# Kernel tuning notes

Measured on AMD Instinct MI355X. Metric: run time of the kernel, lower is better.

## Reference

```python
import jax, jax.numpy as jnp
import numpy as np

N_SAMPLES = 4194304
N_RAYS = 131072


def setup_inputs() -> dict:
    key = jax.random.key(0)
    k1, k2, k3, k4, k5, k6 = jax.random.split(key, 6)
    alpha = jax.random.uniform(k1, (N_SAMPLES, 1), dtype=jnp.float32)
    values3d = jax.random.uniform(k2, (N_SAMPLES, 3), dtype=jnp.float32)
    values1d = jax.random.uniform(k3, (N_SAMPLES, 1), dtype=jnp.float32)
    weights = jax.random.uniform(k4, (N_SAMPLES, 1), dtype=jnp.float32)
    sample_values = jax.random.normal(k5, (N_SAMPLES, 3), dtype=jnp.float32)
    ray_id = jnp.sort(jax.random.randint(k6, (N_SAMPLES,), 0, N_RAYS, dtype=jnp.int32))
    return {"alpha": alpha, "values3d": values3d, "values1d": values1d,
            "weights": weights, "sample_values": sample_values,
            "ray_id": ray_id, "n_rays": N_RAYS}


def _transmittance(alpha, ray_id, n_rays):
    # exclusive cumprod of (1 - alpha) within each packed ray segment, in log space
    logs = jnp.log(jnp.clip(1.0 - alpha[:, 0], 1e-7, 1.0))          # [N]
    csum = jnp.cumsum(logs)
    excl = csum - logs                                               # exclusive cumsum
    first = jnp.concatenate([jnp.ones((1,), bool), ray_id[1:] != ray_id[:-1]])
    seg_base = jax.ops.segment_sum(jnp.where(first, excl, 0.0), ray_id,
                                   num_segments=n_rays)              # [R]
    transmittance = jnp.exp(excl - seg_base[ray_id])[:, None]        # [N,1]
    bg_transmittance = jnp.exp(jax.ops.segment_sum(logs, ray_id,
                                                   num_segments=n_rays))  # [R]
    return transmittance, bg_transmittance


def reference(alpha, values3d, values1d, weights, sample_values, ray_id, n_rays):
    transmittance, bg_transmittance = _transmittance(alpha, ray_id, n_rays)
    # integrate_3d / integrate_1d: per-ray sum of value * weight
    integrated_3d = jax.ops.segment_sum(values3d * weights, ray_id, num_segments=n_rays)  # [R,3]
    integrated_1d = jax.ops.segment_sum(values1d * weights, ray_id, num_segments=n_rays)  # [R,1]
    # SumOverRay: per-ray sum plus broadcast back to each sample
    sum_per_ray = jax.ops.segment_sum(sample_values, ray_id, num_segments=n_rays)         # [R,3]
    sum_per_sample = sum_per_ray[ray_id]                                                  # [N,3]
    return (transmittance, bg_transmittance, integrated_3d, integrated_1d,
            sum_per_ray, sum_per_sample)
```

## Files before the change

### kernel.cpp

```cpp
#include <hip/hip_runtime.h>

typedef float f32x4 __attribute__((ext_vector_type(4)));

template<int CTRL>
__device__ __forceinline__ float dpp1(float x) {
    return __int_as_float(__builtin_amdgcn_update_dpp(
        0x3f800000, __float_as_int(x), CTRL, 0xF, 0xF, false));
}
template<int CTRL>
__device__ __forceinline__ float dpp0(float x) {
    return __int_as_float(__builtin_amdgcn_update_dpp(
        0, __float_as_int(x), CTRL, 0xF, 0xF, true));
}
template<int PAT>
__device__ __forceinline__ float swz(float x) {
    return __int_as_float(__builtin_amdgcn_ds_swizzle(__float_as_int(x), PAT));
}
#define FUNNEL16(v) do { \
    v += dpp0<0x111>(v); \
    v += dpp0<0x112>(v); \
    v += dpp0<0x114>(v); \
    v += dpp0<0x118>(v); } while (0)

__device__ __forceinline__ void ntst4(float* p, float x, float y, float z, float w) {
    f32x4 v = {x, y, z, w};
    __builtin_nontemporal_store(v, (f32x4*)p);
}
__device__ __forceinline__ float sel3(int m, float x, float y, float z) {
    return m == 0 ? x : (m == 1 ? y : z);
}

__global__ __launch_bounds__(256) void seg_bounds_kernel(
    const int* __restrict__ ray_id, int n, int R, int* __restrict__ seg_se)
{
    const int t = blockIdx.x * blockDim.x + threadIdx.x;
    const int a = t * 4;
    if (a >= n) return;
    const int4 rv = *(const int4*)(ray_id + a);

#define TRANS(u, v, p) do {                                                   \
        if ((u) >= 0) seg_se[2 * (u) + 1] = (p);                              \
        for (int id_ = (u) + 1; id_ < (v); ++id_) {                           \
            seg_se[2 * id_] = (p); seg_se[2 * id_ + 1] = (p); }               \
        if ((v) < R) seg_se[2 * (v)] = (p); } while (0)

    if (a == 0) TRANS(-1, rv.x, 0);
    if (rv.y != rv.x) TRANS(rv.x, rv.y, a + 1);
    if (rv.z != rv.y) TRANS(rv.y, rv.z, a + 2);
    if (rv.w != rv.z) TRANS(rv.z, rv.w, a + 3);
    if (a + 4 == n) {
        TRANS(rv.w, R, n);
    } else {
        const int nx = ray_id[a + 4];
        if (nx != rv.w) TRANS(rv.w, nx, a + 4);
    }
#undef TRANS
}

__global__ __launch_bounds__(512) void ray_kernel(
    const float* __restrict__ alpha,
    const float* __restrict__ values3d,
    const float* __restrict__ values1d,
    const float* __restrict__ weights,
    const float* __restrict__ sample_values,
    const int*   __restrict__ seg_se,
    float* __restrict__ out_T,
    float* __restrict__ out_bg,
    float* __restrict__ out_i3,
    float* __restrict__ out_i1,
    float* __restrict__ out_spr,
    float* __restrict__ out_sps,
    int R)
{
    __shared__ float prr[32][9];

    const int lane = threadIdx.x & 63;
    const int wid  = threadIdx.x >> 6;
    const int j    = lane & 15;
    const int g    = lane >> 4;
    const int slot = wid * 4 + g;
    const int r0   = blockIdx.x * 32;
    const int r    = r0 + slot;
    const bool ray_ok = (r < R);
    const int rc = ray_ok ? r : 0;

    const int2 se = ((const int2*)seg_se)[rc];
    int s0 = se.x, s1 = se.y;
    if (!ray_ok) { s0 = 0; s1 = 0; }

    float c = 1.0f;
    float i3x = 0.f, i3y = 0.f, i3z = 0.f, i1 = 0.f;
    float sx = 0.f, sy = 0.f, sz = 0.f;

    const int base0 = s0 & ~3;

    for (int base = base0; base < s1; base += 64) {
        const int a = base + 4 * j;
        const bool tile_ok = (a < s1);
        const int  al = tile_ok ? a : base0;

        const f32x4 av  = *(const f32x4*)(alpha + al);
        const f32x4 wv  = *(const f32x4*)(weights + al);
        const f32x4 v1v = *(const f32x4*)(values1d + al);
        const f32x4 b0  = *(const f32x4*)(values3d + 3 * al);
        const f32x4 b1  = *(const f32x4*)(values3d + 3 * al + 4);
        const f32x4 b2  = *(const f32x4*)(values3d + 3 * al + 8);
        const f32x4 q0  = *(const f32x4*)(sample_values + 3 * al);
        const f32x4 q1  = *(const f32x4*)(sample_values + 3 * al + 4);
        const f32x4 q2  = *(const f32x4*)(sample_values + 3 * al + 8);

        const bool w0 = tile_ok & (a + 0 >= s0);
        const bool w1 = tile_ok & (a + 1 >= s0) & (a + 1 < s1);
        const bool w2 = tile_ok & (a + 2 >= s0) & (a + 2 < s1);
        const bool w3 = tile_ok & (a + 3 < s1);

        float o0 = fminf(fmaxf(1.0f - av.x, 1e-7f), 1.0f); if (!w0) o0 = 1.0f;
        float o1 = fminf(fmaxf(1.0f - av.y, 1e-7f), 1.0f); if (!w1) o1 = 1.0f;
        float o2 = fminf(fmaxf(1.0f - av.z, 1e-7f), 1.0f); if (!w2) o2 = 1.0f;
        float o3 = fminf(fmaxf(1.0f - av.w, 1e-7f), 1.0f); if (!w3) o3 = 1.0f;

        const float p01  = o0 * o1;
        const float p012 = p01 * o2;
        float p = p012 * o3;

        p *= dpp1<0x111>(p);
        p *= dpp1<0x112>(p);
        p *= dpp1<0x114>(p);
        p *= dpp1<0x118>(p);
        const float gincl = p;
        const float gexcl = dpp1<0x111>(gincl);

        const float cg = c * gexcl;
        const float t0 = cg;
        const float t1 = cg * o0;
        const float t2 = cg * p01;
        const float t3 = cg * p012;

        const float W0 = w0 ? wv.x : 0.f;
        const float W1 = w1 ? wv.y : 0.f;
        const float W2 = w2 ? wv.z : 0.f;
        const float W3 = w3 ? wv.w : 0.f;
        const float M0 = w0 ? 1.f : 0.f;
        const float M1 = w1 ? 1.f : 0.f;
        const float M2 = w2 ? 1.f : 0.f;
        const float M3 = w3 ? 1.f : 0.f;

        i1  += v1v.x * W0 + v1v.y * W1 + v1v.z * W2 + v1v.w * W3;
        i3x += b0.x * W0 + b0.w * W1 + b1.z * W2 + b2.y * W3;
        i3y += b0.y * W0 + b1.x * W1 + b1.w * W2 + b2.z * W3;
        i3z += b0.z * W0 + b1.y * W1 + b2.x * W2 + b2.w * W3;
        sx  += q0.x * M0 + q0.w * M1 + q1.z * M2 + q2.y * M3;
        sy  += q0.y * M0 + q1.x * M1 + q1.w * M2 + q2.z * M3;
        sz  += q0.z * M0 + q1.y * M1 + q2.x * M2 + q2.w * M3;

        if (w0 & w1 & w2 & w3) {
            ntst4(out_T + a, t0, t1, t2, t3);
        } else {
            if (w0) out_T[a + 0] = t0;
            if (w1) out_T[a + 1] = t1;
            if (w2) out_T[a + 2] = t2;
            if (w3) out_T[a + 3] = t3;
        }

        c *= swz<0x1F0>(gincl);
    }

    FUNNEL16(sx);  FUNNEL16(sy);  FUNNEL16(sz);
    sx = swz<0x1F0>(sx);
    sy = swz<0x1F0>(sy);
    sz = swz<0x1F0>(sz);

    {
        const int F0 = 3 * s0, F1 = 3 * s1;
        const int H1 = min((F0 + 3) & ~3, F1);
        const int A1 = max(F1 & ~3, H1);
        if (j < 6) {
            const int f = (j < 3) ? (F0 + j) : (A1 + j - 3);
            const bool doit = (j < 3) ? (f < H1) : (f < F1);
            if (doit) out_sps[f] = sel3(f % 3, sx, sy, sz);
        }
        for (int f = H1 + 4 * j; f < A1; f += 64) {
            const int m = f % 3;
            const float v0 = sel3(m, sx, sy, sz);
            const float v1 = sel3(m == 2 ? 0 : m + 1, sx, sy, sz);
            const float v2 = sel3(m == 0 ? 2 : m - 1, sx, sy, sz);
            ntst4(out_sps + f, v0, v1, v2, v0);
        }
    }

    FUNNEL16(i3x); FUNNEL16(i3y); FUNNEL16(i3z); FUNNEL16(i1);
    if (j == 15) {
        prr[slot][0] = c;
        prr[slot][1] = i1;
        prr[slot][2] = i3x; prr[slot][3] = i3y; prr[slot][4] = i3z;
        prr[slot][5] = sx;  prr[slot][6] = sy;  prr[slot][7] = sz;
    }
    __syncthreads();

    {
        const int t = threadIdx.x;
        if (t < 256) {
            float val; float* addr; int ridx;
            if (t < 32)       { ridx = t;                 val = prr[ridx][0];          addr = out_bg  + r0 + t; }
            else if (t < 64)  { ridx = t - 32;            val = prr[ridx][1];          addr = out_i1  + r0 + ridx; }
            else if (t < 160) { int s = t - 64;  ridx = s / 3; val = prr[ridx][2 + s % 3]; addr = out_i3  + 3 * r0 + s; }
            else              { int s = t - 160; ridx = s / 3; val = prr[ridx][5 + s % 3]; addr = out_spr + 3 * r0 + s; }
            if (r0 + ridx < R) *addr = val;
        }
    }
}

extern "C" void kernel_launch(void* const* d_in, const int* in_sizes, int n_in,
                              void* d_out, int out_size, void* d_ws, size_t ws_size,
                              hipStream_t stream) {
    const float* alpha = (const float*)d_in[0];
    const float* v3    = (const float*)d_in[1];
    const float* v1    = (const float*)d_in[2];
    const float* w     = (const float*)d_in[3];
    const float* sv    = (const float*)d_in[4];
    const int*   rid   = (const int*)d_in[5];

    int N = in_sizes[0];
    int R = (out_size - 4 * N) / 8;

    int* seg_se = (int*)d_ws;

    float* out     = (float*)d_out;
    float* out_T   = out;
    float* out_bg  = out + N;
    float* out_i3  = out_bg + R;
    float* out_i1  = out_i3 + 3 * (size_t)R;
    float* out_spr = out_i1 + R;
    float* out_sps = out_spr + 3 * (size_t)R;

    const int nquad = N / 4;
    seg_bounds_kernel<<<(nquad + 255) / 256, 256, 0, stream>>>(rid, N, R, seg_se);

    int blocks = (R + 31) / 32;
    ray_kernel<<<blocks, 512, 0, stream>>>(alpha, v3, v1, w, sv, seg_se,
                                           out_T, out_bg, out_i3, out_i1, out_spr,
                                           out_sps, R);
}
```

Before: 45.37 us.

## Assign 8 lanes per ray instead of 16 to cut idle lanes

Result: slower. 50.25 us (+10.8%).

```diff
diff --git a/kernel.cpp b/kernel.cpp
--- a/kernel.cpp
+++ b/kernel.cpp
@@ -16,11 +16,6 @@
 __device__ __forceinline__ float swz(float x) {
     return __int_as_float(__builtin_amdgcn_ds_swizzle(__float_as_int(x), PAT));
 }
-#define FUNNEL16(v) do { \
-    v += dpp0<0x111>(v); \
-    v += dpp0<0x112>(v); \
-    v += dpp0<0x114>(v); \
-    v += dpp0<0x118>(v); } while (0)
 
 __device__ __forceinline__ void ntst4(float* p, float x, float y, float z, float w) {
     f32x4 v = {x, y, z, w};
@@ -72,14 +67,14 @@
     float* __restrict__ out_sps,
     int R)
 {
-    __shared__ float prr[32][9];
+    __shared__ float prr[64][9];
 
     const int lane = threadIdx.x & 63;
     const int wid  = threadIdx.x >> 6;
-    const int j    = lane & 15;
-    const int g    = lane >> 4;
-    const int slot = wid * 4 + g;
-    const int r0   = blockIdx.x * 32;
+    const int jj   = lane & 7;
+    const int g    = lane >> 3;
+    const int slot = wid * 8 + g;
+    const int r0   = blockIdx.x * 64;
     const int r    = r0 + slot;
     const bool ray_ok = (r < R);
     const int rc = ray_ok ? r : 0;
@@ -94,8 +89,8 @@
 
     const int base0 = s0 & ~3;
 
-    for (int base = base0; base < s1; base += 64) {
-        const int a = base + 4 * j;
+    for (int base = base0; base < s1; base += 32) {
+        const int a = base + 4 * jj;
         const bool tile_ok = (a < s1);
         const int  al = tile_ok ? a : base0;
 
@@ -123,12 +118,13 @@
         const float p012 = p01 * o2;
         float p = p012 * o3;
 
-        p *= dpp1<0x111>(p);
-        p *= dpp1<0x112>(p);
-        p *= dpp1<0x114>(p);
-        p *= dpp1<0x118>(p);
+        float u;
+        u = dpp1<0x111>(p); p *= (jj >= 1) ? u : 1.0f;
+        u = dpp1<0x112>(p); p *= (jj >= 2) ? u : 1.0f;
+        u = dpp1<0x114>(p); p *= (jj >= 4) ? u : 1.0f;
         const float gincl = p;
-        const float gexcl = dpp1<0x111>(gincl);
+        u = dpp1<0x111>(gincl);
+        const float gexcl = (jj >= 1) ? u : 1.0f;
 
         const float cg = c * gexcl;
         const float t0 = cg;
@@ -162,24 +158,30 @@
             if (w3) out_T[a + 3] = t3;
         }
 
-        c *= swz<0x1F0>(gincl);
-    }
-
-    FUNNEL16(sx);  FUNNEL16(sy);  FUNNEL16(sz);
-    sx = swz<0x1F0>(sx);
-    sy = swz<0x1F0>(sy);
-    sz = swz<0x1F0>(sz);
+        c *= swz<0x00F8>(gincl);
+    }
+
+#define FUNNEL8(v) do { \
+        float u_; \
+        u_ = dpp0<0x111>(v); v += (jj >= 1) ? u_ : 0.f; \
+        u_ = dpp0<0x112>(v); v += (jj >= 2) ? u_ : 0.f; \
+        u_ = dpp0<0x114>(v); v += (jj >= 4) ? u_ : 0.f; } while (0)
+
+    FUNNEL8(sx); FUNNEL8(sy); FUNNEL8(sz);
+    sx = swz<0x00F8>(sx);
+    sy = swz<0x00F8>(sy);
+    sz = swz<0x00F8>(sz);
 
     {
         const int F0 = 3 * s0, F1 = 3 * s1;
         const int H1 = min((F0 + 3) & ~3, F1);
         const int A1 = max(F1 & ~3, H1);
-        if (j < 6) {
-            const int f = (j < 3) ? (F0 + j) : (A1 + j - 3);
-            const bool doit = (j < 3) ? (f < H1) : (f < F1);
+        if (jj < 6) {
+            const int f = (jj < 3) ? (F0 + jj) : (A1 + jj - 3);
+            const bool doit = (jj < 3) ? (f < H1) : (f < F1);
             if (doit) out_sps[f] = sel3(f % 3, sx, sy, sz);
         }
-        for (int f = H1 + 4 * j; f < A1; f += 64) {
+        for (int f = H1 + 4 * jj; f < A1; f += 32) {
             const int m = f % 3;
             const float v0 = sel3(m, sx, sy, sz);
             const float v1 = sel3(m == 2 ? 0 : m + 1, sx, sy, sz);
@@ -188,8 +190,9 @@
         }
     }
 
-    FUNNEL16(i3x); FUNNEL16(i3y); FUNNEL16(i3z); FUNNEL16(i1);
-    if (j == 15) {
+    FUNNEL8(i3x); FUNNEL8(i3y); FUNNEL8(i3z); FUNNEL8(i1);
+#undef FUNNEL8
+    if (jj == 7) {
         prr[slot][0] = c;
         prr[slot][1] = i1;
         prr[slot][2] = i3x; prr[slot][3] = i3y; prr[slot][4] = i3z;
@@ -199,14 +202,12 @@
 
     {
         const int t = threadIdx.x;
-        if (t < 256) {
-            float val; float* addr; int ridx;
-            if (t < 32)       { ridx = t;                 val = prr[ridx][0];          addr = out_bg  + r0 + t; }
-            else if (t < 64)  { ridx = t - 32;            val = prr[ridx][1];          addr = out_i1  + r0 + ridx; }
-            else if (t < 160) { int s = t - 64;  ridx = s / 3; val = prr[ridx][2 + s % 3]; addr = out_i3  + 3 * r0 + s; }
-            else              { int s = t - 160; ridx = s / 3; val = prr[ridx][5 + s % 3]; addr = out_spr + 3 * r0 + s; }
-            if (r0 + ridx < R) *addr = val;
-        }
+        float val; float* addr; int ridx;
+        if (t < 64)       { ridx = t;                 val = prr[ridx][0];          addr = out_bg  + r0 + t; }
+        else if (t < 128) { ridx = t - 64;            val = prr[ridx][1];          addr = out_i1  + r0 + ridx; }
+        else if (t < 320) { int s = t - 128; ridx = s / 3; val = prr[ridx][2 + s % 3]; addr = out_i3  + 3 * r0 + s; }
+        else              { int s = t - 320; ridx = s / 3; val = prr[ridx][5 + s % 3]; addr = out_spr + 3 * r0 + s; }
+        if (r0 + ridx < R) *addr = val;
     }
 }
 
@@ -236,7 +237,7 @@
     const int nquad = N / 4;
     seg_bounds_kernel<<<(nquad + 255) / 256, 256, 0, stream>>>(rid, N, R, seg_se);
 
-    int blocks = (R + 31) / 32;
+    int blocks = (R + 63) / 64;
     ray_kernel<<<blocks, 512, 0, stream>>>(alpha, v3, v1, w, sv, seg_se,
                                            out_T, out_bg, out_i3, out_i1, out_spr,
                                            out_sps, R);
```

## Fuse segment-bound computation into ray kernel via binary search and LDS

Applied to the files above, without the earlier changes.

New measurement: 60.12 us. 32.5% more time.

```diff
diff --git a/kernel.cpp b/kernel.cpp
--- a/kernel.cpp
+++ b/kernel.cpp
@@ -28,33 +28,6 @@
 }
 __device__ __forceinline__ float sel3(int m, float x, float y, float z) {
     return m == 0 ? x : (m == 1 ? y : z);
-}
-
-__global__ __launch_bounds__(256) void seg_bounds_kernel(
-    const int* __restrict__ ray_id, int n, int R, int* __restrict__ seg_se)
-{
-    const int t = blockIdx.x * blockDim.x + threadIdx.x;
-    const int a = t * 4;
-    if (a >= n) return;
-    const int4 rv = *(const int4*)(ray_id + a);
-
-#define TRANS(u, v, p) do {                                                   \
-        if ((u) >= 0) seg_se[2 * (u) + 1] = (p);                              \
-        for (int id_ = (u) + 1; id_ < (v); ++id_) {                           \
-            seg_se[2 * id_] = (p); seg_se[2 * id_ + 1] = (p); }               \
-        if ((v) < R) seg_se[2 * (v)] = (p); } while (0)
-
-    if (a == 0) TRANS(-1, rv.x, 0);
-    if (rv.y != rv.x) TRANS(rv.x, rv.y, a + 1);
-    if (rv.z != rv.y) TRANS(rv.y, rv.z, a + 2);
-    if (rv.w != rv.z) TRANS(rv.z, rv.w, a + 3);
-    if (a + 4 == n) {
-        TRANS(rv.w, R, n);
-    } else {
-        const int nx = ray_id[a + 4];
-        if (nx != rv.w) TRANS(rv.w, nx, a + 4);
-    }
-#undef TRANS
 }
 
 __global__ __launch_bounds__(512) void ray_kernel(
@@ -63,30 +36,53 @@
     const float* __restrict__ values1d,
     const float* __restrict__ weights,
     const float* __restrict__ sample_values,
-    const int*   __restrict__ seg_se,
+    const int*   __restrict__ ray_id,
     float* __restrict__ out_T,
     float* __restrict__ out_bg,
     float* __restrict__ out_i3,
     float* __restrict__ out_i1,
     float* __restrict__ out_spr,
     float* __restrict__ out_sps,
-    int R)
+    int R, int N)
 {
     __shared__ float prr[32][9];
-
-    const int lane = threadIdx.x & 63;
-    const int wid  = threadIdx.x >> 6;
+    __shared__ int lbs[33];
+    __shared__ int win[2];
+
+    const int t  = threadIdx.x;
+    const int r0 = blockIdx.x * 32;
+
+    if (t < 33) lbs[t] = -1;
+    if (t < 2) {
+        const int target = r0 + 32 * t;
+        int lo = 0, hi = N;
+        while (lo < hi) {
+            const int mid = (lo + hi) >> 1;
+            if (ray_id[mid] < target) lo = mid + 1; else hi = mid;
+        }
+        win[t] = lo;
+    }
+    __syncthreads();
+    const int p0 = win[0], p1 = win[1];
+
+    for (int i = p0 + t; i < p1; i += 512) {
+        const int cur  = ray_id[i];
+        const int prev = (i == 0) ? -1 : ray_id[i - 1];
+        const int klo = max(prev + 1, r0);
+        const int khi = min(cur, r0 + 31);
+        for (int k = klo; k <= khi; ++k) lbs[k - r0] = i;
+    }
+    __syncthreads();
+
+    const int lane = t & 63;
+    const int wid  = t >> 6;
     const int j    = lane & 15;
     const int g    = lane >> 4;
     const int slot = wid * 4 + g;
-    const int r0   = blockIdx.x * 32;
     const int r    = r0 + slot;
-    const bool ray_ok = (r < R);
-    const int rc = ray_ok ? r : 0;
-
-    const int2 se = ((const int2*)seg_se)[rc];
-    int s0 = se.x, s1 = se.y;
-    if (!ray_ok) { s0 = 0; s1 = 0; }
+
+    int s0 = lbs[slot];     if (s0 < 0) s0 = p1;
+    int s1 = lbs[slot + 1]; if (s1 < 0) s1 = p1;
 
     float c = 1.0f;
     float i3x = 0.f, i3y = 0.f, i3z = 0.f, i1 = 0.f;
@@ -198,7 +194,6 @@
     __syncthreads();
 
     {
-        const int t = threadIdx.x;
         if (t < 256) {
             float val; float* addr; int ridx;
             if (t < 32)       { ridx = t;                 val = prr[ridx][0];          addr = out_bg  + r0 + t; }
@@ -223,8 +218,6 @@
     int N = in_sizes[0];
     int R = (out_size - 4 * N) / 8;
 
-    int* seg_se = (int*)d_ws;
-
     float* out     = (float*)d_out;
     float* out_T   = out;
     float* out_bg  = out + N;
@@ -233,11 +226,8 @@
     float* out_spr = out_i1 + R;
     float* out_sps = out_spr + 3 * (size_t)R;
 
-    const int nquad = N / 4;
-    seg_bounds_kernel<<<(nquad + 255) / 256, 256, 0, stream>>>(rid, N, R, seg_se);
-
     int blocks = (R + 31) / 32;
-    ray_kernel<<<blocks, 512, 0, stream>>>(alpha, v3, v1, w, sv, seg_se,
+    ray_kernel<<<blocks, 512, 0, stream>>>(alpha, v3, v1, w, sv, rid,
                                            out_T, out_bg, out_i3, out_i1, out_spr,
-                                           out_sps, R);
-}
+                                           out_sps, R, N);
+}
```
